# Kernel optimization log

Measured on AMD Instinct MI355X. Metric: run time of the kernel, lower is better.

Reference implementation:

```python
import jax, jax.numpy as jnp
import numpy as np

N_NODES = 50000
IN_F, HID_F, OUT_F = 256, 128, 40
N_EDGES = 800000


def _uniform(key, shape, scale):
    return jax.random.uniform(key, shape, dtype=jnp.float32, minval=-scale, maxval=scale)


def setup_inputs() -> dict:
    key = jax.random.key(0)
    ks = jax.random.split(key, 20)
    x = jax.random.normal(ks[0], (N_NODES, IN_F), dtype=jnp.float32)
    edge_index = jax.random.randint(ks[1], (2, N_EDGES), 0, N_NODES, dtype=jnp.int64)
    s0, sa0 = 1.0 / np.sqrt(HID_F), 1.0  # std_att = 1/sqrt(1)
    s1, sa1 = 1.0 / np.sqrt(OUT_F), 1.0
    sv = 1.0 / np.sqrt(3.0)
    return {
        "x": x, "edge_index": edge_index,
        "Wl0": _uniform(ks[2], (IN_F, HID_F), s0),
        "Wh0": _uniform(ks[3], (IN_F, HID_F), s0),
        "Wm0": _uniform(ks[4], (IN_F, HID_F), s0),
        "al0": _uniform(ks[5], (HID_F, 1), sa0),
        "ah0": _uniform(ks[6], (HID_F, 1), sa0),
        "am0": _uniform(ks[7], (HID_F, 1), sa0),
        "att0": _uniform(ks[8], (3, 3), sv),
        "Wl1": _uniform(ks[9], (HID_F, OUT_F), s1),
        "Wh1": _uniform(ks[10], (HID_F, OUT_F), s1),
        "Wm1": _uniform(ks[11], (HID_F, OUT_F), s1),
        "al1": _uniform(ks[12], (OUT_F, 1), sa1),
        "ah1": _uniform(ks[13], (OUT_F, 1), sa1),
        "am1": _uniform(ks[14], (OUT_F, 1), sa1),
        "att1": _uniform(ks[15], (3, 3), sv),
    }


def _acm_layer(x, row, col, d_inv, Wl, Wh, Wm, al, ah, am, att):
    n = x.shape[0]
    hl, hh, hm = x @ Wl, x @ Wh, x @ Wm
    # adj_low @ M  with adj_low = D^{-1}(I + A): gather sources, scatter-add to rows
    def low(M):
        return d_inv[:, None] * (M + jax.ops.segment_sum(M[col], row, num_segments=n))
    out_low = jax.nn.relu(low(hl))
    out_high = jax.nn.relu(hh - low(hh))  # adj_high = I - adj_low
    out_mlp = jax.nn.relu(hm)
    T = 3.0
    sig = jax.nn.sigmoid(jnp.concatenate([out_low @ al, out_high @ ah, out_mlp @ am], axis=1))  # [n,3]
    a = jax.nn.softmax((sig @ att) / T, axis=1)
    return 3.0 * (a[:, 0:1] * out_low + a[:, 1:2] * out_high + a[:, 2:3] * out_mlp)


def reference(x, edge_index, Wl0, Wh0, Wm0, al0, ah0, am0, att0,
              Wl1, Wh1, Wm1, al1, ah1, am1, att1):
    n = x.shape[0]
    row, col = edge_index[0], edge_index[1]
    deg = jax.ops.segment_sum(jnp.ones_like(row, dtype=jnp.float32), row, num_segments=n)
    rowsum = 1.0 + deg  # rowsum of I + A (duplicates counted, as in scipy)
    d_inv = jnp.where(rowsum > 0, 1.0 / rowsum, 0.0)
    h = _acm_layer(x, row, col, d_inv, Wl0, Wh0, Wm0, al0, ah0, am0, att0)
    out = _acm_layer(h, row, col, d_inv, Wl1, Wh1, Wm1, al1, ah1, am1, att1)
    return out
```

## Files before the change

kernel.cpp:

```cpp
#include <hip/hip_runtime.h>
#include <math.h>

#define N_NODES 50000
#define N_EDGES 800000
#define IN_F    256
#define HID_F   128
#define OUT_F   40
#define W0N     (3*HID_F)
#define W1N     (3*OUT_F)
#define NB      ((N_NODES + 255) / 256)

#define SEG     128
#define EPB     (N_EDGES / SEG)
#define NWORD   (N_NODES / 2)
#define WB      ((NWORD + 255) / 256)

#define XB   ((N_NODES * IN_F) / (256 * 16))
#define P0B  ((IN_F * W0N) / 256)
#define P1B  ((HID_F * W1N) / 256)
#define HPB0 (SEG)
#define HPB1 (SEG + XB)
#define HPB2 (SEG + XB + P0B)
#define HPREPB (SEG + XB + P0B + P1B)

typedef __attribute__((ext_vector_type(8))) unsigned short ushort8;
typedef __attribute__((ext_vector_type(4))) unsigned short ushort4v;
typedef __attribute__((ext_vector_type(8))) __bf16 bf16x8;
typedef __attribute__((ext_vector_type(4))) float f32x4;
typedef __attribute__((ext_vector_type(2))) float f32x2;

static __device__ __forceinline__ float sigmoidf_(float x) {
    return 1.0f / (1.0f + expf(-x));
}

static __device__ __forceinline__ unsigned short f2bf(float f) {
    unsigned u = __float_as_uint(f);
    u += 0x7FFFu + ((u >> 16) & 1u);
    return (unsigned short)(u >> 16);
}

static __device__ __forceinline__ float bflo(unsigned u) { return __uint_as_float(u << 16); }
static __device__ __forceinline__ float bfhi(unsigned u) { return __uint_as_float(u & 0xffff0000u); }
static __device__ __forceinline__ int rfl(int v) { return __builtin_amdgcn_readfirstlane(v); }


__global__ __launch_bounds__(256) void k_hp(
        const int* __restrict__ ei, unsigned* __restrict__ segHist,
        unsigned short* __restrict__ rank, unsigned* __restrict__ rc,
        const float* __restrict__ x, unsigned short* __restrict__ xb,
        const float* __restrict__ Wl0, const float* __restrict__ Wh0,
        const float* __restrict__ Wm0, unsigned short* __restrict__ W0t,
        const float* __restrict__ Wl1, const float* __restrict__ Wh1,
        const float* __restrict__ Wm1, unsigned short* __restrict__ W1t) {
    __shared__ unsigned hist[NWORD];
    int b = blockIdx.x, t = threadIdx.x;
    if (b < SEG) {
        int seg = b;
        for (int i = t; i < NWORD; i += 256) hist[i] = 0;
        __syncthreads();
        int base = seg * EPB;
        for (int k = t; k < EPB; k += 256) {
            int e = base + k;
            int r = ei[e];
            int c = ei[N_EDGES + e];
            unsigned old = atomicAdd(&hist[r >> 1], (r & 1) ? 0x10000u : 1u);
            unsigned lr = (r & 1) ? (old >> 16) : (old & 0xffffu);
            rank[e] = (unsigned short)lr;
            rc[e] = ((unsigned)r << 16) | (unsigned)c;
        }
        __syncthreads();
        unsigned* dst = segHist + (size_t)seg * NWORD;
        for (int i = t; i < NWORD; i += 256) dst[i] = hist[i];
    } else if (b < HPB1) {
        size_t idx = (size_t)(b - HPB0) * 4096 + t * 16;
        float4 f0 = *(const float4*)(x + idx);
        float4 f1 = *(const float4*)(x + idx + 4);
        float4 f2 = *(const float4*)(x + idx + 8);
        float4 f3 = *(const float4*)(x + idx + 12);
        ushort8 u0, u1;
        u0[0]=f2bf(f0.x); u0[1]=f2bf(f0.y); u0[2]=f2bf(f0.z); u0[3]=f2bf(f0.w);
        u0[4]=f2bf(f1.x); u0[5]=f2bf(f1.y); u0[6]=f2bf(f1.z); u0[7]=f2bf(f1.w);
        u1[0]=f2bf(f2.x); u1[1]=f2bf(f2.y); u1[2]=f2bf(f2.z); u1[3]=f2bf(f2.w);
        u1[4]=f2bf(f3.x); u1[5]=f2bf(f3.y); u1[6]=f2bf(f3.z); u1[7]=f2bf(f3.w);
        *(ushort8*)(xb + idx)     = u0;
        *(ushort8*)(xb + idx + 8) = u1;
    } else if (b < HPB2) {
        int i = (b - HPB1) * 256 + t;
        int n = i / IN_F, k = i % IN_F;
        float v;
        if (n < HID_F)            v = Wl0[k * HID_F + n];
        else if (n < 2 * HID_F)   v = Wh0[k * HID_F + (n - HID_F)];
        else                      v = Wm0[k * HID_F + (n - 2 * HID_F)];
        W0t[i] = f2bf(v);
    } else {
        int i = (b - HPB2) * 256 + t;
        int n = i / HID_F, kp = i % HID_F;
        int k = ((kp >> 6) << 6) + ((kp & 3) << 4) + ((kp >> 2) & 15);
        float v;
        if (n < OUT_F)            v = Wl1[k * OUT_F + n];
        else if (n < 2 * OUT_F)   v = Wh1[k * OUT_F + (n - OUT_F)];
        else                      v = Wm1[k * OUT_F + (n - 2 * OUT_F)];
        W1t[i] = f2bf(v);
    }
}


__global__ __launch_bounds__(256) void k_scanseg(
        unsigned* __restrict__ segHist, int* __restrict__ rowPtr,
        float* __restrict__ dinv, int* __restrict__ blkTot) {
    __shared__ int s[256];
    int t = threadIdx.x;
    int w = blockIdx.x * 256 + t;
    int cum0 = 0, cum1 = 0;
    if (w < NWORD) {
        for (int sg = 0; sg < SEG; ++sg) {
            size_t idx = (size_t)sg * NWORD + w;
            unsigned h = segHist[idx];
            segHist[idx] = ((unsigned)cum1 << 16) | (unsigned)cum0;
            cum0 += (int)(h & 0xffffu);
            cum1 += (int)(h >> 16);
        }
    }
    int deg0 = cum0, deg1 = cum1;
    int pair = deg0 + deg1;
    s[t] = pair; __syncthreads();
    for (int d = 1; d < 256; d <<= 1) {
        int x = (t >= d) ? s[t - d] : 0;
        __syncthreads();
        s[t] += x;
        __syncthreads();
    }
    int basep = s[t] - pair;
    if (w < NWORD) {
        rowPtr[2 * w]     = basep;
        rowPtr[2 * w + 1] = basep + deg0;
        dinv[2 * w]     = 1.0f / (1.0f + (float)deg0);
        dinv[2 * w + 1] = 1.0f / (1.0f + (float)deg1);
    }
    if (t == 255) blkTot[blockIdx.x] = s[255];
}

__global__ void k_scan2(int* __restrict__ blk) {
    __shared__ int s[256];
    int t = threadIdx.x;
    int v = (t < WB) ? blk[t] : 0;
    s[t] = v; __syncthreads();
    for (int d = 1; d < 256; d <<= 1) {
        int x = (t >= d) ? s[t - d] : 0;
        __syncthreads();
        s[t] += x;
        __syncthreads();
    }
    if (t < WB) blk[t] = s[t] - v;
}

__global__ void k_scan3(const int* __restrict__ blkOff, int* __restrict__ rowPtr) {
    int t = threadIdx.x;
    int gid = blockIdx.x * 256 + t;
    if (gid < N_NODES) rowPtr[gid] += blkOff[gid >> 9];
    if (gid == 0) rowPtr[N_NODES] = N_EDGES;
}


#define BKP 40

template<int EPI>
__global__ __launch_bounds__(256) void k_gemm_fill(
        const unsigned short* __restrict__ A, const unsigned short* __restrict__ Bt,
        unsigned short* __restrict__ C0, int ld0,
        unsigned short* __restrict__ C1, int ld1, int nsplit,
        unsigned char* __restrict__ Cq,
        unsigned short* __restrict__ Hs, unsigned char* __restrict__ Hq,
        unsigned short* __restrict__ HmP,
        int M, int N, int K, int nxt,
        const unsigned* __restrict__ rc, const unsigned short* __restrict__ rank,
        const int* __restrict__ rowPtr, const unsigned short* __restrict__ segOff,
        unsigned short* __restrict__ colIdx) {
    __shared__ unsigned short As[128 * BKP];
    __shared__ unsigned short Bs[128 * BKP];
    int tid  = threadIdx.x;

    if ((int)blockIdx.x >= nxt) {
        int fid = (blockIdx.x - nxt) * gridDim.y + blockIdx.y;
        int e = fid * 256 + tid;
        if (e < N_EDGES) {
            unsigned x = rc[e];
            int r = (int)(x >> 16);
            int seg = e / EPB;
            int pos = rowPtr[r] + (int)segOff[(size_t)seg * N_NODES + r] + (int)rank[e];
            colIdx[pos] = (unsigned short)(x & 0xffffu);
        }
        return;
    }

    int lane = tid & 63, wid = tid >> 6;
    int wr = wid >> 1, wc = wid & 1;
    int bm = blockIdx.y * 128, bn = blockIdx.x * 128;

    int srow = tid >> 1;
    int scol = (tid & 1) * 16;

    int garow = min(bm + srow, M - 1);
    int gbrow = min(bn + srow, N - 1);

    f32x4 acc[4][4];
#pragma unroll
    for (int m = 0; m < 4; ++m)
#pragma unroll
        for (int n = 0; n < 4; ++n)
            acc[m][n] = (f32x4)(0.0f);

    int kg = (lane >> 4) * 8;
    int rA = wr * 64 + (lane & 15);
    int rB = wc * 64 + (lane & 15);

    for (int k0 = 0; k0 < K; k0 += 32) {
        {
            const unsigned short* src = A + (size_t)garow * K + k0 + scol;
            *(ushort8*)&As[srow * BKP + scol]     = *(const ushort8*)(src);
            *(ushort8*)&As[srow * BKP + scol + 8] = *(const ushort8*)(src + 8);
        }
        {
            const unsigned short* src = Bt + (size_t)gbrow * K + k0 + scol;
            *(ushort8*)&Bs[srow * BKP + scol]     = *(const ushort8*)(src);
            *(ushort8*)&Bs[srow * BKP + scol + 8] = *(const ushort8*)(src + 8);
        }
        __syncthreads();

        bf16x8 a[4], b[4];
#pragma unroll
        for (int m = 0; m < 4; ++m)
            a[m] = __builtin_bit_cast(bf16x8, *(const ushort8*)&As[(rA + m * 16) * BKP + kg]);
#pragma unroll
        for (int n = 0; n < 4; ++n)
            b[n] = __builtin_bit_cast(bf16x8, *(const ushort8*)&Bs[(rB + n * 16) * BKP + kg]);
#pragma unroll
        for (int m = 0; m < 4; ++m)
#pragma unroll
            for (int n = 0; n < 4; ++n)
                acc[m][n] = __builtin_amdgcn_mfma_f32_16x16x32_bf16(a[m], b[n], acc[m][n], 0, 0, 0);
        __syncthreads();
    }

    int col  = lane & 15;
    int rsub = (lane >> 4) * 4;

    if (EPI == 0) {
#pragma unroll
        for (int m = 0; m < 4; ++m) {
            int gm0 = bm + wr * 64 + m * 16 + rsub;
#pragma unroll
            for (int n = 0; n < 4; ++n) {
                int gn = bn + wc * 64 + n * 16 + col;
                if (gn >= N) continue;
#pragma unroll
                for (int j = 0; j < 4; ++j) {
                    int gm = gm0 + j;
                    if (gm >= M) continue;
                    float v = acc[m][n][j];
                    unsigned short b = f2bf(v);
                    if (gn < nsplit) {
                        C0[(size_t)gm * ld0 + gn] = b;
                        int pk = __builtin_amdgcn_cvt_pk_fp8_f32(v, v, 0, false);
                        Cq[(size_t)gm * nsplit + gn] = (unsigned char)(pk & 0xff);
                    } else {
                        C1[(size_t)gm * ld1 + (gn - nsplit)] = b;
                    }
                }
            }
        }
    } else {
#pragma unroll
        for (int m = 0; m < 4; ++m) {
            int gm0 = bm + wr * 64 + m * 16 + rsub;
#pragma unroll
            for (int j = 0; j < 4; ++j) {
                int gm = gm0 + j;
                if (gm >= M) continue;
                float v0 = acc[m][0][j], v1 = acc[m][1][j];
                float v2 = acc[m][2][j], v3 = acc[m][3][j];
                ushort4v o;
                o[0] = f2bf(v0); o[1] = f2bf(v1); o[2] = f2bf(v2); o[3] = f2bf(v3);
                if (bn < 256) {
                    int pos = bn + wc * 64 + col * 4;
                    *(ushort4v*)&Hs[(size_t)gm * 256 + pos] = o;
                    int pk = 0;
                    pk = __builtin_amdgcn_cvt_pk_fp8_f32(v0, v1, pk, false);
                    pk = __builtin_amdgcn_cvt_pk_fp8_f32(v2, v3, pk, true);
                    *(unsigned*)&Hq[(size_t)gm * 256 + pos] = (unsigned)pk;
                } else {
                    int pos = wc * 64 + col * 4;
                    *(ushort4v*)&HmP[(size_t)gm * 128 + pos] = o;
                }
            }
        }
    }
}


__global__ __launch_bounds__(256) void k_layer0(
        const unsigned short* __restrict__ Hs, const unsigned char* __restrict__ Hq,
        const unsigned short* __restrict__ HmP,
        const int* __restrict__ rowPtr, const unsigned short* __restrict__ colIdx,
        const float* __restrict__ dinv,
        const float* __restrict__ al, const float* __restrict__ ah,
        const float* __restrict__ am, const float* __restrict__ att,
        unsigned short* __restrict__ hout) {
    int lane = threadIdx.x & 63;
    int i = blockIdx.x * 4 + (threadIdx.x >> 6);

    int p0 = rfl(rowPtr[i]);
    int p1 = rfl(rowPtr[i + 1]);
    int deg = p1 - p0;
    float a0 = 0.f, a1 = 0.f, a2 = 0.f, a3 = 0.f;
    int off4 = lane * 4;

    auto gath = [&](int js) -> unsigned {
        return *(const unsigned*)(Hq + ((size_t)(unsigned)js << 8) + off4);
    };
    auto addw = [&](unsigned w) {
        f32x2 d0 = __builtin_amdgcn_cvt_pk_f32_fp8((int)w, false);
        f32x2 d1 = __builtin_amdgcn_cvt_pk_f32_fp8((int)w, true);
        a0 += d0.x; a1 += d0.y; a2 += d1.x; a3 += d1.y;
    };

    for (int c = 0; c < deg; c += 64) {
        int rem = deg - c; if (rem > 64) rem = 64;
        int mycol = (int)colIdx[p0 + c + (lane < rem ? lane : 0)];
        int q = 0;
        for (; q + 7 < rem; q += 8) {
            int j0 = rfl(__shfl(mycol, q + 0));
            int j1 = rfl(__shfl(mycol, q + 1));
            int j2 = rfl(__shfl(mycol, q + 2));
            int j3 = rfl(__shfl(mycol, q + 3));
            int j4 = rfl(__shfl(mycol, q + 4));
            int j5 = rfl(__shfl(mycol, q + 5));
            int j6 = rfl(__shfl(mycol, q + 6));
            int j7 = rfl(__shfl(mycol, q + 7));
            unsigned w0 = gath(j0), w1 = gath(j1), w2 = gath(j2), w3 = gath(j3);
            unsigned w4 = gath(j4), w5 = gath(j5), w6 = gath(j6), w7 = gath(j7);
            addw(w0); addw(w1); addw(w2); addw(w3);
            addw(w4); addw(w5); addw(w6); addw(w7);
        }
        for (; q < rem; ++q) {
            int j = rfl(__shfl(mycol, q));
            addw(gath(j));
        }
    }

    uint2 sv = *(const uint2*)(Hs + (size_t)i * 256 + off4);
    float s0 = bflo(sv.x), s1 = bfhi(sv.x), s2 = bflo(sv.y), s3 = bfhi(sv.y);
    float di = dinv[i];
    float l0 = di * (s0 + a0), l1 = di * (s1 + a1);
    float l2 = di * (s2 + a2), l3 = di * (s3 + a3);

    float ol0 = fmaxf(l0, 0.f), ol1 = fmaxf(l1, 0.f);
    float ol2 = fmaxf(l2, 0.f), ol3 = fmaxf(l3, 0.f);
    float oh0 = fmaxf(s0 - l0, 0.f), oh1 = fmaxf(s1 - l1, 0.f);
    float oh2 = fmaxf(s2 - l2, 0.f), oh3 = fmaxf(s3 - l3, 0.f);

    int c0 = ((lane >> 4) << 6) + (lane & 15);

    float om0 = 0.f, om1 = 0.f, om2 = 0.f, om3 = 0.f;
    float prA, prM = 0.f;
    if (lane < 32) {
        uint2 hv = *(const uint2*)(HmP + (size_t)i * 128 + off4);
        om0 = fmaxf(bflo(hv.x), 0.f); om1 = fmaxf(bfhi(hv.x), 0.f);
        om2 = fmaxf(bflo(hv.y), 0.f); om3 = fmaxf(bfhi(hv.y), 0.f);
        prA = ol0 * al[c0] + ol1 * al[c0 + 16] + ol2 * al[c0 + 32] + ol3 * al[c0 + 48];
        prM = om0 * am[c0] + om1 * am[c0 + 16] + om2 * am[c0 + 32] + om3 * am[c0 + 48];
    } else {
        int ch = c0 - 128;
        prA = oh0 * ah[ch] + oh1 * ah[ch + 16] + oh2 * ah[ch + 32] + oh3 * ah[ch + 48];
    }

#pragma unroll
    for (int d = 1; d < 32; d <<= 1) prA += __shfl_xor(prA, d);
#pragma unroll
    for (int d = 1; d < 32; d <<= 1) prM += __shfl_xor(prM, d);
    float g0 = __shfl(prA, 0);
    float g1 = __shfl(prA, 32);
    float g2 = __shfl(prM, 0);

    float sg0 = sigmoidf_(g0), sg1 = sigmoidf_(g1), sg2 = sigmoidf_(g2);
    const float inv3 = (1.0f / 3.0f);
    float e0 = (sg0 * att[0] + sg1 * att[3] + sg2 * att[6]) * inv3;
    float e1 = (sg0 * att[1] + sg1 * att[4] + sg2 * att[7]) * inv3;
    float e2 = (sg0 * att[2] + sg1 * att[5] + sg2 * att[8]) * inv3;
    float mx = fmaxf(e0, fmaxf(e1, e2));
    float x0 = expf(e0 - mx), x1 = expf(e1 - mx), x2 = expf(e2 - mx);
    float inv = 1.0f / (x0 + x1 + x2);
    float c0f = 3.0f * inv * x0, c1f = 3.0f * inv * x1, c2f = 3.0f * inv * x2;

    int src = lane | 32;
    float th0 = __shfl(oh0, src), th1 = __shfl(oh1, src);
    float th2 = __shfl(oh2, src), th3 = __shfl(oh3, src);

    if (lane < 32) {
        ushort4v o;
        o[0] = f2bf(c0f * ol0 + c1f * th0 + c2f * om0);
        o[1] = f2bf(c0f * ol1 + c1f * th1 + c2f * om1);
        o[2] = f2bf(c0f * ol2 + c1f * th2 + c2f * om2);
        o[3] = f2bf(c0f * ol3 + c1f * th3 + c2f * om3);
        *(ushort4v*)&hout[(size_t)i * 128 + off4] = o;
    }
}


__global__ __launch_bounds__(256) void k_layer1(
        const unsigned short* __restrict__ H1g, const unsigned char* __restrict__ H1q,
        const unsigned short* __restrict__ H1m,
        const int* __restrict__ rowPtr, const unsigned short* __restrict__ colIdx,
        const float* __restrict__ dinv,
        const float* __restrict__ al, const float* __restrict__ ah,
        const float* __restrict__ am, const float* __restrict__ att,
        float* __restrict__ out) {
    int lane = threadIdx.x & 63;
    int i = blockIdx.x * 4 + (threadIdx.x >> 6);

    int p0 = rfl(rowPtr[i]);
    int p1 = rfl(rowPtr[i + 1]);
    int deg = p1 - p0;
    float a0 = 0.f, a1 = 0.f, a2 = 0.f, a3 = 0.f;
    bool active = lane < 20;
    int off4 = lane * 4;
    int offc = active ? off4 : 0;

    auto gath = [&](int js) -> unsigned {
        return *(const unsigned*)(H1q + (size_t)((unsigned)js * 80u) + offc);
    };
    auto addw = [&](unsigned w) {
        f32x2 d0 = __builtin_amdgcn_cvt_pk_f32_fp8((int)w, false);
        f32x2 d1 = __builtin_amdgcn_cvt_pk_f32_fp8((int)w, true);
        a0 += d0.x; a1 += d0.y; a2 += d1.x; a3 += d1.y;
    };

    for (int c = 0; c < deg; c += 64) {
        int rem = deg - c; if (rem > 64) rem = 64;
        int mycol = (int)colIdx[p0 + c + (lane < rem ? lane : 0)];
        int q = 0;
        for (; q + 7 < rem; q += 8) {
            int j0 = rfl(__shfl(mycol, q + 0));
            int j1 = rfl(__shfl(mycol, q + 1));
            int j2 = rfl(__shfl(mycol, q + 2));
            int j3 = rfl(__shfl(mycol, q + 3));
            int j4 = rfl(__shfl(mycol, q + 4));
            int j5 = rfl(__shfl(mycol, q + 5));
            int j6 = rfl(__shfl(mycol, q + 6));
            int j7 = rfl(__shfl(mycol, q + 7));
            unsigned w0 = gath(j0), w1 = gath(j1), w2 = gath(j2), w3 = gath(j3);
            unsigned w4 = gath(j4), w5 = gath(j5), w6 = gath(j6), w7 = gath(j7);
            addw(w0); addw(w1); addw(w2); addw(w3);
            addw(w4); addw(w5); addw(w6); addw(w7);
        }
        for (; q < rem; ++q) {
            int j = rfl(__shfl(mycol, q));
            addw(gath(j));
        }
    }

    float s0 = 0.f, s1 = 0.f, s2 = 0.f, s3 = 0.f;
    if (active) {
        uint2 sv = *(const uint2*)(H1g + (size_t)i * 80 + off4);
        s0 = bflo(sv.x); s1 = bfhi(sv.x); s2 = bflo(sv.y); s3 = bfhi(sv.y);
    }
    float di = dinv[i];
    float l0 = di * (s0 + a0), l1 = di * (s1 + a1);
    float l2 = di * (s2 + a2), l3 = di * (s3 + a3);

    float ol0 = fmaxf(l0, 0.f), ol1 = fmaxf(l1, 0.f);
    float ol2 = fmaxf(l2, 0.f), ol3 = fmaxf(l3, 0.f);
    float oh0 = fmaxf(s0 - l0, 0.f), oh1 = fmaxf(s1 - l1, 0.f);
    float oh2 = fmaxf(s2 - l2, 0.f), oh3 = fmaxf(s3 - l3, 0.f);

    float om0 = 0.f, om1 = 0.f, om2 = 0.f, om3 = 0.f;
    float r0 = 0.f, r1 = 0.f, r2 = 0.f;
    if (lane < 10) {
        uint2 hv = *(const uint2*)(H1m + (size_t)i * 40 + off4);
        om0 = fmaxf(bflo(hv.x), 0.f); om1 = fmaxf(bfhi(hv.x), 0.f);
        om2 = fmaxf(bflo(hv.y), 0.f); om3 = fmaxf(bfhi(hv.y), 0.f);
        float4 alv = *(const float4*)(al + off4);
        float4 amv = *(const float4*)(am + off4);
        r0 = ol0 * alv.x + ol1 * alv.y + ol2 * alv.z + ol3 * alv.w;
        r2 = om0 * amv.x + om1 * amv.y + om2 * amv.z + om3 * amv.w;
    } else if (lane < 20) {
        float4 ahv = *(const float4*)(ah + (off4 - 40));
        r1 = oh0 * ahv.x + oh1 * ahv.y + oh2 * ahv.z + oh3 * ahv.w;
    }

#pragma unroll
    for (int d = 1; d < 64; d <<= 1) r0 += __shfl_xor(r0, d);
#pragma unroll
    for (int d = 1; d < 64; d <<= 1) r1 += __shfl_xor(r1, d);
#pragma unroll
    for (int d = 1; d < 64; d <<= 1) r2 += __shfl_xor(r2, d);

    float sg0 = sigmoidf_(r0), sg1 = sigmoidf_(r1), sg2 = sigmoidf_(r2);
    const float inv3 = (1.0f / 3.0f);
    float e0 = (sg0 * att[0] + sg1 * att[3] + sg2 * att[6]) * inv3;
    float e1 = (sg0 * att[1] + sg1 * att[4] + sg2 * att[7]) * inv3;
    float e2 = (sg0 * att[2] + sg1 * att[5] + sg2 * att[8]) * inv3;
    float mx = fmaxf(e0, fmaxf(e1, e2));
    float x0 = expf(e0 - mx), x1 = expf(e1 - mx), x2 = expf(e2 - mx);
    float inv = 1.0f / (x0 + x1 + x2);
    float c0 = 3.0f * inv * x0, c1 = 3.0f * inv * x1, c2 = 3.0f * inv * x2;

    int src = (lane + 10) & 63;
    float th0 = __shfl(oh0, src), th1 = __shfl(oh1, src);
    float th2 = __shfl(oh2, src), th3 = __shfl(oh3, src);

    if (lane < 10) {
        float4 o;
        o.x = c0 * ol0 + c1 * th0 + c2 * om0;
        o.y = c0 * ol1 + c1 * th1 + c2 * om1;
        o.z = c0 * ol2 + c1 * th2 + c2 * om2;
        o.w = c0 * ol3 + c1 * th3 + c2 * om3;
        *(float4*)&out[(size_t)i * 40 + off4] = o;
    }
}


extern "C" void kernel_launch(void* const* d_in, const int* in_sizes, int n_in,
                              void* d_out, int out_size, void* d_ws, size_t ws_size,
                              hipStream_t stream) {
    const float* x    = (const float*)d_in[0];
    const int*   ei   = (const int*)d_in[1];
    const float* Wl0  = (const float*)d_in[2];
    const float* Wh0  = (const float*)d_in[3];
    const float* Wm0  = (const float*)d_in[4];
    const float* al0  = (const float*)d_in[5];
    const float* ah0  = (const float*)d_in[6];
    const float* am0  = (const float*)d_in[7];
    const float* att0 = (const float*)d_in[8];
    const float* Wl1  = (const float*)d_in[9];
    const float* Wh1  = (const float*)d_in[10];
    const float* Wm1  = (const float*)d_in[11];
    const float* al1  = (const float*)d_in[12];
    const float* ah1  = (const float*)d_in[13];
    const float* am1  = (const float*)d_in[14];
    const float* att1 = (const float*)d_in[15];
    float* out = (float*)d_out;

    char* ws = (char*)d_ws;
    size_t off = 0;
    auto alloc = [&](size_t bytes) -> char* {
        char* p = ws + off;
        off += (bytes + 255) & ~(size_t)255;
        return p;
    };
    int*      rowPtr  = (int*)     alloc((size_t)(N_NODES + 1) * 4);
    int*      blkTot  = (int*)     alloc(256 * 4);
    unsigned* segHist = (unsigned*)alloc((size_t)SEG * NWORD * 4);
    unsigned short* rank   = (unsigned short*)alloc((size_t)N_EDGES * 2);
    unsigned*       rc     = (unsigned*)      alloc((size_t)N_EDGES * 4);
    unsigned short* colIdx = (unsigned short*)alloc((size_t)N_EDGES * 2 + 256);
    float* dinv   = (float*)alloc((size_t)N_NODES * 4);
    unsigned short* W0t  = (unsigned short*)alloc((size_t)W0N * IN_F * 2);
    unsigned short* W1t  = (unsigned short*)alloc((size_t)W1N * HID_F * 2);
    unsigned short* xb   = (unsigned short*)alloc((size_t)N_NODES * IN_F * 2);
    unsigned short* Hs   = (unsigned short*)alloc((size_t)N_NODES * 256 * 2);
    unsigned char*  Hq   = (unsigned char*) alloc((size_t)N_NODES * 256);
    unsigned short* HmP  = (unsigned short*)alloc((size_t)N_NODES * 128 * 2);
    unsigned short* H1g  = (unsigned short*)alloc((size_t)N_NODES * 80 * 2);
    unsigned char*  H1q  = (unsigned char*) alloc((size_t)N_NODES * 80 + 256);
    unsigned short* H1m  = (unsigned short*)alloc((size_t)N_NODES * 40 * 2);
    unsigned short* hbuf = (unsigned short*)alloc((size_t)N_NODES * HID_F * 2);

    k_hp<<<HPREPB, 256, 0, stream>>>(ei, segHist, rank, rc,
                                     x, xb, Wl0, Wh0, Wm0, W0t,
                                     Wl1, Wh1, Wm1, W1t);
    k_scanseg<<<WB, 256, 0, stream>>>(segHist, rowPtr, dinv, blkTot);
    k_scan2<<<1, 256, 0, stream>>>(blkTot);
    k_scan3<<<NB, 256, 0, stream>>>(blkTot, rowPtr);
    {
        dim3 grid(3 + 8, (N_NODES + 127) / 128);
        k_gemm_fill<1><<<grid, 256, 0, stream>>>(xb, W0t,
                                                 nullptr, 0, nullptr, 0, 0, nullptr,
                                                 Hs, Hq, HmP,
                                                 N_NODES, W0N, IN_F, 3,
                                                 rc, rank, rowPtr,
                                                 (const unsigned short*)segHist, colIdx);
    }
    k_layer0<<<N_NODES / 4, 256, 0, stream>>>(Hs, Hq, HmP, rowPtr, colIdx, dinv,
                                              al0, ah0, am0, att0, hbuf);
    {
        dim3 grid(1, (N_NODES + 127) / 128);
        k_gemm_fill<0><<<grid, 256, 0, stream>>>(hbuf, W1t,
                                                 H1g, 80, H1m, 40, 80, H1q,
                                                 nullptr, nullptr, nullptr,
                                                 N_NODES, W1N, HID_F, 1,
                                                 nullptr, nullptr, nullptr, nullptr, nullptr);
    }
    k_layer1<<<N_NODES / 4, 256, 0, stream>>>(H1g, H1q, H1m, rowPtr, colIdx, dinv,
                                              al1, ah1, am1, att1, out);
}
```

Baseline: 189.6 us.

## Prefetch GEMM tiles into registers and split layer0 node work across two waves

In the GEMM, the global loads for the next K tile are issued into registers right after the barrier, so they overlap the MFMA work on the current tile. Layer0 now gives each node two wavefronts, one for the low half and one for the high half of the features, each gathering 2 bytes per lane instead of 4. The halves exchange the high-branch result through shared memory and a block barrier. This doubles the waves in flight for the latency-bound gather, at the cost of extra shared-memory traffic, a barrier, and idle half-waves during the final combine.

```diff
diff --git a/kernel.cpp b/kernel.cpp
--- a/kernel.cpp
+++ b/kernel.cpp
@@ -214,18 +214,25 @@
     int rA = wr * 64 + (lane & 15);
     int rB = wc * 64 + (lane & 15);
 
+    const unsigned short* srcA = A + (size_t)garow * K + scol;
+    const unsigned short* srcB = Bt + (size_t)gbrow * K + scol;
+    ushort8 ra0 = *(const ushort8*)(srcA);
+    ushort8 ra1 = *(const ushort8*)(srcA + 8);
+    ushort8 rb0 = *(const ushort8*)(srcB);
+    ushort8 rb1 = *(const ushort8*)(srcB + 8);
+
     for (int k0 = 0; k0 < K; k0 += 32) {
-        {
-            const unsigned short* src = A + (size_t)garow * K + k0 + scol;
-            *(ushort8*)&As[srow * BKP + scol]     = *(const ushort8*)(src);
-            *(ushort8*)&As[srow * BKP + scol + 8] = *(const ushort8*)(src + 8);
-        }
-        {
-            const unsigned short* src = Bt + (size_t)gbrow * K + k0 + scol;
-            *(ushort8*)&Bs[srow * BKP + scol]     = *(const ushort8*)(src);
-            *(ushort8*)&Bs[srow * BKP + scol + 8] = *(const ushort8*)(src + 8);
-        }
-        __syncthreads();
+        *(ushort8*)&As[srow * BKP + scol]     = ra0;
+        *(ushort8*)&As[srow * BKP + scol + 8] = ra1;
+        *(ushort8*)&Bs[srow * BKP + scol]     = rb0;
+        *(ushort8*)&Bs[srow * BKP + scol + 8] = rb1;
+        __syncthreads();
+        if (k0 + 32 < K) {
+            ra0 = *(const ushort8*)(srcA + k0 + 32);
+            ra1 = *(const ushort8*)(srcA + k0 + 40);
+            rb0 = *(const ushort8*)(srcB + k0 + 32);
+            rb1 = *(const ushort8*)(srcB + k0 + 40);
+        }
 
         bf16x8 a[4], b[4];
 #pragma unroll
@@ -307,21 +314,26 @@
         const float* __restrict__ am, const float* __restrict__ att,
         unsigned short* __restrict__ hout) {
     int lane = threadIdx.x & 63;
-    int i = blockIdx.x * 4 + (threadIdx.x >> 6);
+    int wid  = threadIdx.x >> 6;
+    int half = wid & 1;
+    int node = wid >> 1;
+    int i = blockIdx.x * 2 + node;
+
+    __shared__ float ohBuf[2][64][2];
+    __shared__ float g1s[2];
 
     int p0 = rfl(rowPtr[i]);
     int p1 = rfl(rowPtr[i + 1]);
     int deg = p1 - p0;
-    float a0 = 0.f, a1 = 0.f, a2 = 0.f, a3 = 0.f;
-    int off4 = lane * 4;
-
+    int off2 = half * 128 + lane * 2;
+
+    float a0 = 0.f, a1 = 0.f;
     auto gath = [&](int js) -> unsigned {
-        return *(const unsigned*)(Hq + ((size_t)(unsigned)js << 8) + off4);
+        return (unsigned)*(const unsigned short*)(Hq + ((size_t)(unsigned)js << 8) + off2);
     };
     auto addw = [&](unsigned w) {
-        f32x2 d0 = __builtin_amdgcn_cvt_pk_f32_fp8((int)w, false);
-        f32x2 d1 = __builtin_amdgcn_cvt_pk_f32_fp8((int)w, true);
-        a0 += d0.x; a1 += d0.y; a2 += d1.x; a3 += d1.y;
+        f32x2 d = __builtin_amdgcn_cvt_pk_f32_fp8((int)w, false);
+        a0 += d.x; a1 += d.y;
     };
 
     for (int c = 0; c < deg; c += 64) {
@@ -348,61 +360,55 @@
         }
     }
 
-    uint2 sv = *(const uint2*)(Hs + (size_t)i * 256 + off4);
-    float s0 = bflo(sv.x), s1 = bfhi(sv.x), s2 = bflo(sv.y), s3 = bfhi(sv.y);
+    unsigned sv = *(const unsigned*)(Hs + (size_t)i * 256 + half * 128 + lane * 2);
+    float s0 = bflo(sv), s1 = bfhi(sv);
     float di = dinv[i];
     float l0 = di * (s0 + a0), l1 = di * (s1 + a1);
-    float l2 = di * (s2 + a2), l3 = di * (s3 + a3);
-
-    float ol0 = fmaxf(l0, 0.f), ol1 = fmaxf(l1, 0.f);
-    float ol2 = fmaxf(l2, 0.f), ol3 = fmaxf(l3, 0.f);
-    float oh0 = fmaxf(s0 - l0, 0.f), oh1 = fmaxf(s1 - l1, 0.f);
-    float oh2 = fmaxf(s2 - l2, 0.f), oh3 = fmaxf(s3 - l3, 0.f);
-
-    int c0 = ((lane >> 4) << 6) + (lane & 15);
-
-    float om0 = 0.f, om1 = 0.f, om2 = 0.f, om3 = 0.f;
-    float prA, prM = 0.f;
-    if (lane < 32) {
-        uint2 hv = *(const uint2*)(HmP + (size_t)i * 128 + off4);
-        om0 = fmaxf(bflo(hv.x), 0.f); om1 = fmaxf(bfhi(hv.x), 0.f);
-        om2 = fmaxf(bflo(hv.y), 0.f); om3 = fmaxf(bfhi(hv.y), 0.f);
-        prA = ol0 * al[c0] + ol1 * al[c0 + 16] + ol2 * al[c0 + 32] + ol3 * al[c0 + 48];
-        prM = om0 * am[c0] + om1 * am[c0 + 16] + om2 * am[c0 + 32] + om3 * am[c0 + 48];
+
+    int p = lane * 2;
+    int f0 = ((p >> 6) << 6) + ((p & 3) << 4) + ((p >> 2) & 15);
+
+    float v0, v1, om0 = 0.f, om1 = 0.f, pr, prM = 0.f;
+    if (half == 0) {
+        v0 = fmaxf(l0, 0.f); v1 = fmaxf(l1, 0.f);
+        unsigned hv = *(const unsigned*)(HmP + (size_t)i * 128 + lane * 2);
+        om0 = fmaxf(bflo(hv), 0.f); om1 = fmaxf(bfhi(hv), 0.f);
+        pr  = v0 * al[f0] + v1 * al[f0 + 16];
+        prM = om0 * am[f0] + om1 * am[f0 + 16];
     } else {
-        int ch = c0 - 128;
-        prA = oh0 * ah[ch] + oh1 * ah[ch + 16] + oh2 * ah[ch + 32] + oh3 * ah[ch + 48];
-    }
-
-#pragma unroll
-    for (int d = 1; d < 32; d <<= 1) prA += __shfl_xor(prA, d);
-#pragma unroll
-    for (int d = 1; d < 32; d <<= 1) prM += __shfl_xor(prM, d);
-    float g0 = __shfl(prA, 0);
-    float g1 = __shfl(prA, 32);
-    float g2 = __shfl(prM, 0);
-
-    float sg0 = sigmoidf_(g0), sg1 = sigmoidf_(g1), sg2 = sigmoidf_(g2);
-    const float inv3 = (1.0f / 3.0f);
-    float e0 = (sg0 * att[0] + sg1 * att[3] + sg2 * att[6]) * inv3;
-    float e1 = (sg0 * att[1] + sg1 * att[4] + sg2 * att[7]) * inv3;
-    float e2 = (sg0 * att[2] + sg1 * att[5] + sg2 * att[8]) * inv3;
-    float mx = fmaxf(e0, fmaxf(e1, e2));
-    float x0 = expf(e0 - mx), x1 = expf(e1 - mx), x2 = expf(e2 - mx);
-    float inv = 1.0f / (x0 + x1 + x2);
-    float c0f = 3.0f * inv * x0, c1f = 3.0f * inv * x1, c2f = 3.0f * inv * x2;
-
-    int src = lane | 32;
-    float th0 = __shfl(oh0, src), th1 = __shfl(oh1, src);
-    float th2 = __shfl(oh2, src), th3 = __shfl(oh3, src);
-
-    if (lane < 32) {
-        ushort4v o;
-        o[0] = f2bf(c0f * ol0 + c1f * th0 + c2f * om0);
-        o[1] = f2bf(c0f * ol1 + c1f * th1 + c2f * om1);
-        o[2] = f2bf(c0f * ol2 + c1f * th2 + c2f * om2);
-        o[3] = f2bf(c0f * ol3 + c1f * th3 + c2f * om3);
-        *(ushort4v*)&hout[(size_t)i * 128 + off4] = o;
+        v0 = fmaxf(s0 - l0, 0.f); v1 = fmaxf(s1 - l1, 0.f);
+        pr = v0 * ah[f0] + v1 * ah[f0 + 16];
+    }
+
+#pragma unroll
+    for (int d = 1; d < 64; d <<= 1) pr += __shfl_xor(pr, d);
+#pragma unroll
+    for (int d = 1; d < 64; d <<= 1) prM += __shfl_xor(prM, d);
+
+    if (half == 1) {
+        if (lane == 0) g1s[node] = pr;
+        ohBuf[node][lane][0] = v0;
+        ohBuf[node][lane][1] = v1;
+    }
+    __syncthreads();
+
+    if (half == 0) {
+        float g0 = pr, g2 = prM, g1 = g1s[node];
+        float sg0 = sigmoidf_(g0), sg1 = sigmoidf_(g1), sg2 = sigmoidf_(g2);
+        const float inv3 = (1.0f / 3.0f);
+        float e0 = (sg0 * att[0] + sg1 * att[3] + sg2 * att[6]) * inv3;
+        float e1 = (sg0 * att[1] + sg1 * att[4] + sg2 * att[7]) * inv3;
+        float e2 = (sg0 * att[2] + sg1 * att[5] + sg2 * att[8]) * inv3;
+        float mx = fmaxf(e0, fmaxf(e1, e2));
+        float x0 = expf(e0 - mx), x1 = expf(e1 - mx), x2 = expf(e2 - mx);
+        float inv = 1.0f / (x0 + x1 + x2);
+        float c0f = 3.0f * inv * x0, c1f = 3.0f * inv * x1, c2f = 3.0f * inv * x2;
+
+        float oh0 = ohBuf[node][lane][0];
+        float oh1 = ohBuf[node][lane][1];
+        unsigned o = (unsigned)f2bf(c0f * v0 + c1f * oh0 + c2f * om0)
+                   | ((unsigned)f2bf(c0f * v1 + c1f * oh1 + c2f * om1) << 16);
+        *(unsigned*)&hout[(size_t)i * 128 + lane * 2] = o;
     }
 }
 
@@ -581,7 +587,7 @@
                                                  rc, rank, rowPtr,
                                                  (const unsigned short*)segHist, colIdx);
     }
-    k_layer0<<<N_NODES / 4, 256, 0, stream>>>(Hs, Hq, HmP, rowPtr, colIdx, dinv,
+    k_layer0<<<N_NODES / 2, 256, 0, stream>>>(Hs, Hq, HmP, rowPtr, colIdx, dinv,
                                               al0, ah0, am0, att0, hbuf);
     {
         dim3 grid(1, (N_NODES + 127) / 128);
```

Result: slower. 208.5 us (+9.9%).
